# Kernel tuning notes

Hardware: AMD Instinct MI355X
Metric: run time of the kernel (lower is better)

The kernel has to match this reference:

```python
import jax, jax.numpy as jnp
import numpy as np

N_NODES = 100000
D = 128
N_EDGES = 1000000


def setup_inputs() -> dict:
    key = jax.random.key(0)
    k1, k2, k3 = jax.random.split(key, 3)
    z = jax.random.normal(k1, (N_NODES, D), dtype=jnp.float32)
    edge_index = jax.random.randint(k2, (2, N_EDGES), 0, N_NODES, dtype=jnp.int64)
    # Linear(2*D, 1): weight [1, 2*D], bias [1] (torch convention)
    W = jax.random.normal(k3, (1, 2 * D), dtype=jnp.float32) * (1.0 / np.sqrt(2 * D))
    b = jnp.zeros((1,), dtype=jnp.float32)
    return {"z": z, "edge_index": edge_index, "W": W, "b": b}


def reference(z, edge_index, W, b):
    src = edge_index[0]
    dst = edge_index[1]
    # cat([z[src], z[dst]]) @ W.T == z[src] @ W_src.T + z[dst] @ W_dst.T
    # (split-weight form avoids materializing the [E, 2D] concat)
    W_src = W[:, :D]  # [1, D]
    W_dst = W[:, D:]  # [1, D]
    logits = z[src] @ W_src[0] + z[dst] @ W_dst[0] + b[0]  # [E]
    return jax.nn.sigmoid(logits)
```

## Files before the change

kernel.cpp:

```cpp
#include <hip/hip_runtime.h>
#include <hip/hip_bf16.h>

#define N_NODES 100000
#define D 128
#define N_EDGES 1000000

__global__ void __launch_bounds__(256) node_scores_kernel(
    const float* __restrict__ z, const float* __restrict__ W,
    const float* __restrict__ b, float* __restrict__ s) {
  int tid  = blockIdx.x * blockDim.x + threadIdx.x;
  int wave = tid >> 6;
  int lane = threadIdx.x & 63;
  int sub  = lane >> 4;
  int l16  = lane & 15;
  int node = wave * 4 + sub;

  const float4* zrow = reinterpret_cast<const float4*>(z + (size_t)node * D);
  const float4 z0 = zrow[l16];
  const float4 z1 = zrow[16 + l16];

  const float4* Wv = reinterpret_cast<const float4*>(W);
  const float4 ws0 = Wv[l16],      ws1 = Wv[16 + l16];
  const float4 wd0 = Wv[32 + l16], wd1 = Wv[48 + l16];

  float a = z0.x * ws0.x + z0.y * ws0.y + z0.z * ws0.z + z0.w * ws0.w
          + z1.x * ws1.x + z1.y * ws1.y + z1.z * ws1.z + z1.w * ws1.w;
  float c = z0.x * wd0.x + z0.y * wd0.y + z0.z * wd0.z + z0.w * wd0.w
          + z1.x * wd1.x + z1.y * wd1.y + z1.z * wd1.z + z1.w * wd1.w;

  #pragma unroll
  for (int off = 8; off >= 1; off >>= 1) {
    a += __shfl_xor(a, off, 64);
    c += __shfl_xor(c, off, 64);
  }
  if (l16 == 0) {
    s[node] = a + b[0];
    s[N_NODES + node] = c;
  }
}

__global__ void __launch_bounds__(256) edge_kernel(
    const int* __restrict__ idx, const float* __restrict__ s,
    float* __restrict__ out) {
  int t = blockIdx.x * blockDim.x + threadIdx.x;
  if (t * 2 >= N_EDGES) return;
  const int2 sv = reinterpret_cast<const int2*>(idx)[t];
  const int2 dv = reinterpret_cast<const int2*>(idx + N_EDGES)[t];
  const float* __restrict__ sd = s + N_NODES;

  float l0 = s[sv.x] + sd[dv.x];
  float l1 = s[sv.y] + sd[dv.y];

  float2 o;
  o.x = 1.0f / (1.0f + __expf(-l0));
  o.y = 1.0f / (1.0f + __expf(-l1));
  reinterpret_cast<float2*>(out)[t] = o;
}

extern "C" void kernel_launch(void* const* d_in, const int* in_sizes, int n_in,
                              void* d_out, int out_size, void* d_ws, size_t ws_size,
                              hipStream_t stream) {
  const float* z   = (const float*)d_in[0];
  const int*   idx = (const int*)d_in[1];
  const float* W   = (const float*)d_in[2];
  const float* b   = (const float*)d_in[3];
  float* out = (float*)d_out;
  float* s   = (float*)d_ws;

  node_scores_kernel<<<N_NODES / 16, 256, 0, stream>>>(z, W, b, s);

  int blocks2 = (N_EDGES / 2 + 255) / 256;
  edge_kernel<<<blocks2, 256, 0, stream>>>(idx, s, out);
}
```

Baseline: 24.74 us.

## Interleave node scores, widen per-lane node work, use nontemporal edge I/O

The node-score kernel now gives each node 8 lanes instead of 16, so each lane loads four float4 chunks and a wave covers 8 nodes. The launch uses half as many blocks. The src and dst scores are stored interleaved as a float2 per node rather than as two separate arrays, and the edge kernel indexes into that interleaved layout. Edge index loads and output stores use nontemporal builtins to avoid polluting the cache, which leaves more room for the gathered scores. Interleaving means each score gather touches a table twice as wide, which may reduce cache locality, since src and dst lookups hit different nodes.

```diff
diff --git a/kernel.cpp b/kernel.cpp
--- a/kernel.cpp
+++ b/kernel.cpp
@@ -5,56 +5,70 @@
 #define D 128
 #define N_EDGES 1000000
 
-__global__ void __launch_bounds__(256) node_scores_kernel(
+typedef float v2f __attribute__((ext_vector_type(2)));
+typedef int   v2i __attribute__((ext_vector_type(2)));
+
+__global__ void __launch_bounds__(256, 4) node_scores_kernel(
     const float* __restrict__ z, const float* __restrict__ W,
-    const float* __restrict__ b, float* __restrict__ s) {
-  int tid  = blockIdx.x * blockDim.x + threadIdx.x;
-  int wave = tid >> 6;
-  int lane = threadIdx.x & 63;
-  int sub  = lane >> 4;
-  int l16  = lane & 15;
-  int node = wave * 4 + sub;
+    const float* __restrict__ b, v2f* __restrict__ s2) {
+  const int tid  = blockIdx.x * blockDim.x + threadIdx.x;
+  const int wave = tid >> 6;
+  const int lane = threadIdx.x & 63;
+  const int sub  = lane >> 3;
+  const int l8   = lane & 7;
+  const int node = wave * 8 + sub;
 
   const float4* zrow = reinterpret_cast<const float4*>(z + (size_t)node * D);
-  const float4 z0 = zrow[l16];
-  const float4 z1 = zrow[16 + l16];
+  const float4 z0 = zrow[l8];
+  const float4 z1 = zrow[8 + l8];
+  const float4 z2 = zrow[16 + l8];
+  const float4 z3 = zrow[24 + l8];
 
   const float4* Wv = reinterpret_cast<const float4*>(W);
-  const float4 ws0 = Wv[l16],      ws1 = Wv[16 + l16];
-  const float4 wd0 = Wv[32 + l16], wd1 = Wv[48 + l16];
+  const float4 ws0 = Wv[l8],      ws1 = Wv[8 + l8];
+  const float4 ws2 = Wv[16 + l8], ws3 = Wv[24 + l8];
+  const float4 wd0 = Wv[32 + l8], wd1 = Wv[40 + l8];
+  const float4 wd2 = Wv[48 + l8], wd3 = Wv[56 + l8];
 
   float a = z0.x * ws0.x + z0.y * ws0.y + z0.z * ws0.z + z0.w * ws0.w
-          + z1.x * ws1.x + z1.y * ws1.y + z1.z * ws1.z + z1.w * ws1.w;
+          + z1.x * ws1.x + z1.y * ws1.y + z1.z * ws1.z + z1.w * ws1.w
+          + z2.x * ws2.x + z2.y * ws2.y + z2.z * ws2.z + z2.w * ws2.w
+          + z3.x * ws3.x + z3.y * ws3.y + z3.z * ws3.z + z3.w * ws3.w;
   float c = z0.x * wd0.x + z0.y * wd0.y + z0.z * wd0.z + z0.w * wd0.w
-          + z1.x * wd1.x + z1.y * wd1.y + z1.z * wd1.z + z1.w * wd1.w;
+          + z1.x * wd1.x + z1.y * wd1.y + z1.z * wd1.z + z1.w * wd1.w
+          + z2.x * wd2.x + z2.y * wd2.y + z2.z * wd2.z + z2.w * wd2.w
+          + z3.x * wd3.x + z3.y * wd3.y + z3.z * wd3.z + z3.w * wd3.w;
 
   #pragma unroll
-  for (int off = 8; off >= 1; off >>= 1) {
+  for (int off = 4; off >= 1; off >>= 1) {
     a += __shfl_xor(a, off, 64);
     c += __shfl_xor(c, off, 64);
   }
-  if (l16 == 0) {
-    s[node] = a + b[0];
-    s[N_NODES + node] = c;
+  if (l8 == 0) {
+    v2f st;
+    st.x = a + b[0];
+    st.y = c;
+    s2[node] = st;
   }
 }
 
 __global__ void __launch_bounds__(256) edge_kernel(
-    const int* __restrict__ idx, const float* __restrict__ s,
+    const int* __restrict__ idx, const float* __restrict__ sp,
     float* __restrict__ out) {
   int t = blockIdx.x * blockDim.x + threadIdx.x;
   if (t * 2 >= N_EDGES) return;
-  const int2 sv = reinterpret_cast<const int2*>(idx)[t];
-  const int2 dv = reinterpret_cast<const int2*>(idx + N_EDGES)[t];
-  const float* __restrict__ sd = s + N_NODES;
+  const v2i sv = __builtin_nontemporal_load(
+      reinterpret_cast<const v2i*>(idx) + t);
+  const v2i dv = __builtin_nontemporal_load(
+      reinterpret_cast<const v2i*>(idx + N_EDGES) + t);
 
-  float l0 = s[sv.x] + sd[dv.x];
-  float l1 = s[sv.y] + sd[dv.y];
+  float l0 = sp[2 * sv.x] + sp[2 * dv.x + 1];
+  float l1 = sp[2 * sv.y] + sp[2 * dv.y + 1];
 
-  float2 o;
+  v2f o;
   o.x = 1.0f / (1.0f + __expf(-l0));
   o.y = 1.0f / (1.0f + __expf(-l1));
-  reinterpret_cast<float2*>(out)[t] = o;
+  __builtin_nontemporal_store(o, reinterpret_cast<v2f*>(out) + t);
 }
 
 extern "C" void kernel_launch(void* const* d_in, const int* in_sizes, int n_in,
@@ -65,10 +79,10 @@
   const float* W   = (const float*)d_in[2];
   const float* b   = (const float*)d_in[3];
   float* out = (float*)d_out;
-  float* s   = (float*)d_ws;
+  v2f*   s2  = (v2f*)d_ws;
 
-  node_scores_kernel<<<N_NODES / 16, 256, 0, stream>>>(z, W, b, s);
+  node_scores_kernel<<<N_NODES / 32, 256, 0, stream>>>(z, W, b, s2);
 
   int blocks2 = (N_EDGES / 2 + 255) / 256;
-  edge_kernel<<<blocks2, 256, 0, stream>>>(idx, s, out);
+  edge_kernel<<<blocks2, 256, 0, stream>>>(idx, (const float*)s2, out);
 }
```

After: 24.99 us. Within noise of the previous version (+1.0%).
